# Kernel tuning notes

Hardware: AMD Instinct MI355X
Metric: run time of the kernel (lower is better)

The kernel has to match this reference:

```python
import jax, jax.numpy as jnp
import numpy as np

NODE = 64
T = 256
M = 2048
IN_SCALE = 1.0


def setup_inputs() -> dict:
    key = jax.random.key(0)
    k1, k2, k3, k4 = jax.random.split(key, 4)
    # nn.Linear-like init: small weights so the 255-step recurrence is stable
    W = jax.random.normal(k1, (T, NODE, NODE), dtype=jnp.float32) * 0.06
    b = jax.random.normal(k2, (T, NODE), dtype=jnp.float32) * 0.01
    noise_embedding = jnp.ones((1, NODE, T), dtype=jnp.float32)
    eps0 = jax.random.normal(k3, (M, NODE), dtype=jnp.float32)   # initial rsample noise
    eps = jax.random.normal(k4, (T - 1, M, NODE), dtype=jnp.float32)  # per-step noise, t=1..T-1
    return {"W": W, "b": b, "noise_embedding": noise_embedding, "eps0": eps0, "eps": eps}


def reference(W, b, noise_embedding, eps0, eps):
    m = eps0.shape[0]
    dtype = eps0.dtype
    m0 = jnp.zeros((m, NODE), dtype)
    s0 = jnp.full((m, NODE), IN_SCALE, dtype)
    x0 = s0 * eps0  # Normal(m0, s0).rsample()

    st_all = jax.nn.softplus(noise_embedding[0].T)  # (T, NODE)

    def step(x_prev, inp):
        Wt, bt, st, et = inp
        mt = x_prev @ Wt.T + bt                       # (M, NODE) coupling layer
        s_full = jnp.broadcast_to(st, (m, NODE))      # repeat over batch
        xt = mt + s_full * et
        return xt, (xt, mt, s_full)

    _, (xs, ms, ss) = jax.lax.scan(step, x0, (W[1:], b[1:], st_all[1:], eps))

    def pack(first, rest):
        seq = jnp.concatenate([first[None], rest], axis=0)  # (T, M, NODE), t ascending
        return jnp.flip(seq, axis=0).transpose(1, 2, 0)     # (M, NODE, T), reversed order

    return pack(x0, xs), pack(m0, ms), pack(s0, ss)
```

## Files before the change

### kernel.cpp

```cpp
#include <hip/hip_runtime.h>
#include <cmath>


typedef __bf16 bf16x8 __attribute__((ext_vector_type(8)));
typedef float f32x4 __attribute__((ext_vector_type(4)));

#define XB_STRIDE 144

__device__ __forceinline__ float softplus_f(float z) {
  return (z > 20.0f) ? z : log1pf(expf(z));
}

__global__ void k_wf(const float* __restrict__ W, const float* __restrict__ ne,
                     bf16x8* __restrict__ Wf, float* __restrict__ st,
                     float* __restrict__ stT) {
  int t = blockIdx.x;
  for (int e = threadIdx.x; e < 512; e += blockDim.x) {
    int lane = e & 63;
    int kh = (e >> 6) & 1;
    int nt = e >> 7;
    int q = lane >> 4, n15 = lane & 15;
    int n = nt * 16 + n15;
    int k0 = kh * 32 + q * 8;
    const float* src = W + ((size_t)t * 64 + n) * 64 + k0;
    bf16x8 v;
#pragma unroll
    for (int j = 0; j < 8; ++j) v[j] = (__bf16)src[j];
    Wf[((size_t)(t * 4 + nt) * 2 + kh) * 64 + lane] = v;
  }
  if (threadIdx.x < 64) {
    int n = threadIdx.x;
    float v = (t == 0) ? 1.0f : softplus_f(ne[n * 256 + t]);
    st[n * 256 + t] = v;
    stT[t * 64 + n] = v;
  }
}

__global__ __launch_bounds__(256) void k_prefix(const bf16x8* __restrict__ Wf,
                                                bf16x8* __restrict__ Pf) {
  __shared__ __align__(16) unsigned char Q[64 * XB_STRIDE];
  int b = blockIdx.x;
  int c = b + 1;
  int tid = threadIdx.x;
  int lane = tid & 63, w = tid >> 6;
  int q = lane >> 4, n15 = lane & 15;
  int rbase = w * 16;
  for (int e = tid; e < 4096; e += 256) {
    int r = e >> 6, k = e & 63;
    *(__bf16*)(Q + r * XB_STRIDE + k * 2) = (__bf16)((r == k) ? 1.0f : 0.0f);
  }
  __syncthreads();
  for (int tl = 0; tl < 16; ++tl) {
    int t = c * 16 + tl;
    bf16x8 a0 = *(const bf16x8*)(Q + (rbase + n15) * XB_STRIDE + q * 16);
    bf16x8 a1 = *(const bf16x8*)(Q + (rbase + n15) * XB_STRIDE + 64 + q * 16);
    f32x4 acc[4];
#pragma unroll
    for (int nt = 0; nt < 4; ++nt) {
      bf16x8 b0 = Wf[((size_t)(t * 4 + nt) * 2 + 0) * 64 + lane];
      bf16x8 b1 = Wf[((size_t)(t * 4 + nt) * 2 + 1) * 64 + lane];
      f32x4 z = {0.f, 0.f, 0.f, 0.f};
      z = __builtin_amdgcn_mfma_f32_16x16x32_bf16(a0, b0, z, 0, 0, 0);
      z = __builtin_amdgcn_mfma_f32_16x16x32_bf16(a1, b1, z, 0, 0, 0);
      acc[nt] = z;
    }
#pragma unroll
    for (int nt = 0; nt < 4; ++nt)
#pragma unroll
      for (int reg = 0; reg < 4; ++reg)
        *(__bf16*)(Q + (rbase + 4 * q + reg) * XB_STRIDE + (nt * 16 + n15) * 2) =
            (__bf16)acc[nt][reg];
    __syncthreads();
    for (int e = tid; e < 512; e += 256) {
      int lane2 = e & 63;
      int kh = (e >> 6) & 1;
      int nt = e >> 7;
      int q2 = lane2 >> 4;
      int nn = nt * 16 + (lane2 & 15);
      bf16x8 v;
#pragma unroll
      for (int j = 0; j < 8; ++j)
        v[j] = *(const __bf16*)(Q + (kh * 32 + q2 * 8 + j) * XB_STRIDE + nn * 2);
      Pf[((size_t)(b * 16 + tl) * 8 + nt * 2 + kh) * 64 + lane2] = v;
    }
    __syncthreads();
  }
}

__global__ __launch_bounds__(256) void k_phase1(
    const float* __restrict__ bb, const float* __restrict__ st,
    const float* __restrict__ eps0, const float* __restrict__ eps,
    const bf16x8* __restrict__ Wf, float* __restrict__ xtemp) {
  __shared__ float stab[16][64];
  __shared__ float btab[16][64];
  __shared__ __align__(16) unsigned char xball[4 * 16 * XB_STRIDE];
  int tid = threadIdx.x, w = tid >> 6, lane = tid & 63;
  unsigned char* xb = xball + w * 16 * XB_STRIDE;
  int c = blockIdx.x >> 5;
  int r0 = ((blockIdx.x & 31) * 4 + w) * 16;
  int q = lane >> 4, n15 = lane & 15;
  for (int e = tid; e < 1024; e += 256) {
    int tl = e >> 6, n = e & 63, t = c * 16 + tl;
    stab[tl][n] = st[n * 256 + t];
    btab[tl][n] = bb[t * 64 + n];
  }
  if (c == 0) {
    for (int i = 0; i < 16; ++i) {
      float v = eps0[(size_t)(r0 + i) * 64 + lane];
      *(__bf16*)(xb + i * XB_STRIDE + lane * 2) = (__bf16)v;
      xtemp[((size_t)(r0 + i)) * 64 + lane] = v;
    }
  } else {
    for (int i = 0; i < 16; ++i)
      *(__bf16*)(xb + i * XB_STRIDE + lane * 2) = (__bf16)0.0f;
  }
  __syncthreads();
  int t0 = (c == 0) ? 1 : c * 16;
  int t1 = c * 16 + 15;
  float epc[16], epn[16];
#pragma unroll
  for (int nt = 0; nt < 4; ++nt)
#pragma unroll
    for (int reg = 0; reg < 4; ++reg)
      epc[nt * 4 + reg] =
          eps[((size_t)(t0 - 1) * 2048 + r0 + 4 * q + reg) * 64 + nt * 16 + n15];
  for (int t = t0; t <= t1; ++t) {
    bool more = (t < t1);
    if (more) {
#pragma unroll
      for (int nt = 0; nt < 4; ++nt)
#pragma unroll
        for (int reg = 0; reg < 4; ++reg)
          epn[nt * 4 + reg] =
              eps[((size_t)t * 2048 + r0 + 4 * q + reg) * 64 + nt * 16 + n15];
    }
    bf16x8 a0 = *(const bf16x8*)(xb + n15 * XB_STRIDE + q * 16);
    bf16x8 a1 = *(const bf16x8*)(xb + n15 * XB_STRIDE + 64 + q * 16);
    f32x4 acc[4];
#pragma unroll
    for (int nt = 0; nt < 4; ++nt) {
      bf16x8 b0 = Wf[((size_t)(t * 4 + nt) * 2 + 0) * 64 + lane];
      bf16x8 b1 = Wf[((size_t)(t * 4 + nt) * 2 + 1) * 64 + lane];
      f32x4 z = {0.f, 0.f, 0.f, 0.f};
      z = __builtin_amdgcn_mfma_f32_16x16x32_bf16(a0, b0, z, 0, 0, 0);
      z = __builtin_amdgcn_mfma_f32_16x16x32_bf16(a1, b1, z, 0, 0, 0);
      acc[nt] = z;
    }
    int tl = t - c * 16;
#pragma unroll
    for (int nt = 0; nt < 4; ++nt) {
      int n = nt * 16 + n15;
      float sv = stab[tl][n];
      float bv = btab[tl][n];
#pragma unroll
      for (int reg = 0; reg < 4; ++reg) {
        int row = 4 * q + reg;
        float xn = acc[nt][reg] + bv + sv * epc[nt * 4 + reg];
        xtemp[((size_t)t * 2048 + r0 + row) * 64 + n] = xn;
        *(__bf16*)(xb + row * XB_STRIDE + n * 2) = (__bf16)xn;
      }
    }
    if (more) {
#pragma unroll
      for (int i = 0; i < 16; ++i) epc[i] = epn[i];
    }
  }
}

__global__ __launch_bounds__(256) void k_phase2(const bf16x8* __restrict__ Pf,
                                                const float* __restrict__ xtemp,
                                                bf16x8* __restrict__ hA) {
  __shared__ __align__(16) unsigned char hball[4 * 16 * XB_STRIDE];
  int tid = threadIdx.x, w = tid >> 6, lane = tid & 63;
  unsigned char* hb = hball + w * 16 * XB_STRIDE;
  int rtile = blockIdx.x * 4 + w;
  int r0 = rtile * 16;
  int q = lane >> 4, n15 = lane & 15;
  for (int i = 0; i < 16; ++i) {
    float v = xtemp[((size_t)15 * 2048 + r0 + i) * 64 + lane];
    *(__bf16*)(hb + i * XB_STRIDE + lane * 2) = (__bf16)v;
  }
  for (int c = 1; c <= 15; ++c) {
    bf16x8 a0 = *(const bf16x8*)(hb + n15 * XB_STRIDE + q * 16);
    bf16x8 a1 = *(const bf16x8*)(hb + n15 * XB_STRIDE + 64 + q * 16);
    size_t hbase = ((size_t)(c - 1) * 128 + rtile) * 128;
    hA[hbase + lane] = a0;
    hA[hbase + 64 + lane] = a1;
    if (c == 15) break;
    f32x4 acc[4];
#pragma unroll
    for (int nt = 0; nt < 4; ++nt) {
      bf16x8 b0 = Pf[((size_t)((c - 1) * 16 + 15) * 8 + nt * 2 + 0) * 64 + lane];
      bf16x8 b1 = Pf[((size_t)((c - 1) * 16 + 15) * 8 + nt * 2 + 1) * 64 + lane];
      f32x4 z = {0.f, 0.f, 0.f, 0.f};
      z = __builtin_amdgcn_mfma_f32_16x16x32_bf16(a0, b0, z, 0, 0, 0);
      z = __builtin_amdgcn_mfma_f32_16x16x32_bf16(a1, b1, z, 0, 0, 0);
      acc[nt] = z;
    }
#pragma unroll
    for (int nt = 0; nt < 4; ++nt) {
      int n = nt * 16 + n15;
#pragma unroll
      for (int reg = 0; reg < 4; ++reg) {
        int row = 4 * q + reg;
        float tail = xtemp[((size_t)(16 * c + 15) * 2048 + r0 + row) * 64 + n];
        float hn = acc[nt][reg] + tail;
        *(__bf16*)(hb + row * XB_STRIDE + n * 2) = (__bf16)hn;
      }
    }
  }
}

__global__ __launch_bounds__(256) void k_fix(const bf16x8* __restrict__ Pf,
                                             const bf16x8* __restrict__ hA,
                                             float* __restrict__ xtemp) {
  int tid = threadIdx.x, w = tid >> 6, lane = tid & 63;
  int rtile = (blockIdx.x & 31) * 4 + w;
  int r0 = rtile * 16;
  int ct = blockIdx.x >> 5;
  int c1 = ct >> 4;
  int tl = ct & 15;
  int c = c1 + 1;
  int t = 16 * c + tl;
  int q = lane >> 4, n15 = lane & 15;
  size_t hbase = ((size_t)c1 * 128 + rtile) * 128;
  bf16x8 a0 = hA[hbase + lane];
  bf16x8 a1 = hA[hbase + 64 + lane];
#pragma unroll
  for (int nt = 0; nt < 4; ++nt) {
    bf16x8 b0 = Pf[((size_t)(c1 * 16 + tl) * 8 + nt * 2 + 0) * 64 + lane];
    bf16x8 b1 = Pf[((size_t)(c1 * 16 + tl) * 8 + nt * 2 + 1) * 64 + lane];
    f32x4 z = {0.f, 0.f, 0.f, 0.f};
    z = __builtin_amdgcn_mfma_f32_16x16x32_bf16(a0, b0, z, 0, 0, 0);
    z = __builtin_amdgcn_mfma_f32_16x16x32_bf16(a1, b1, z, 0, 0, 0);
#pragma unroll
    for (int reg = 0; reg < 4; ++reg) {
      size_t idx = ((size_t)t * 2048 + r0 + 4 * q + reg) * 64 + nt * 16 + n15;
      xtemp[idx] += z[reg];
    }
  }
}

__global__ __launch_bounds__(256) void k_pack(const float* __restrict__ stT,
                                              const float* __restrict__ eps0,
                                              const float* __restrict__ eps,
                                              const float* __restrict__ xtemp,
                                              float* __restrict__ out) {
  __shared__ __align__(16) float lds[4][64 * 36];
  int tid = threadIdx.x;
  int w = tid >> 6, lane = tid & 63;
  float* wls = lds[w];
  int task = blockIdx.x * 4 + w;
  int tile = task >> 11;
  int mm = task & 2047;
  int tt0 = tile * 32;
  int iblk0 = 224 - tt0;
  int l15 = lane & 15, L = lane >> 4;
  int n0 = 4 * l15;
  f32x4 xr[8], er[8];
#pragma unroll
  for (int r = 0; r < 8; ++r) {
    int t = tt0 + 4 * r + L;
    xr[r] = *(const f32x4*)(xtemp + ((size_t)t * 2048 + mm) * 64 + n0);
    const float* erow = (t == 0) ? (eps0 + (size_t)mm * 64)
                                 : (eps + ((size_t)(t - 1) * 2048 + mm) * 64);
    er[r] = *(const f32x4*)(erow + n0);
  }
#pragma unroll
  for (int r = 0; r < 8; ++r) {
    int t = tt0 + 4 * r + L;
    f32x4 s = *(const f32x4*)(stT + (size_t)t * 64 + n0);
    er[r] = xr[r] - s * er[r];
  }
  int nrd = lane >> 3;
  int crd = (lane & 7) * 4;
  const size_t MSOFF = (size_t)2048 * 64 * 256;
  size_t obase = ((size_t)mm * 64) * 256 + (size_t)(iblk0 + crd);
#pragma unroll
  for (int r = 0; r < 8; ++r) {
    int col = 31 - 4 * r - L;
#pragma unroll
    for (int j = 0; j < 4; ++j) wls[(n0 + j) * 36 + col] = xr[r][j];
  }
#pragma unroll
  for (int jj = 0; jj < 8; ++jj) {
    int nn = 8 * jj + nrd;
    f32x4 v = *(const f32x4*)(wls + nn * 36 + crd);
    *(f32x4*)(out + obase + (size_t)nn * 256) = v;
  }
#pragma unroll
  for (int r = 0; r < 8; ++r) {
    int col = 31 - 4 * r - L;
#pragma unroll
    for (int j = 0; j < 4; ++j) wls[(n0 + j) * 36 + col] = er[r][j];
  }
#pragma unroll
  for (int jj = 0; jj < 8; ++jj) {
    int nn = 8 * jj + nrd;
    f32x4 v = *(const f32x4*)(wls + nn * 36 + crd);
    *(f32x4*)(out + MSOFF + obase + (size_t)nn * 256) = v;
  }
}

__global__ __launch_bounds__(256) void k_s(const float* __restrict__ st,
                                           float* __restrict__ out) {
  int gid = blockIdx.x * 256 + threadIdx.x;
  int i0 = (gid & 63) * 4;
  int n = (gid >> 6) & 63;
  int m = gid >> 12;
  const float4 rv = *(const float4*)(st + n * 256 + 252 - i0);
  f32x4 v = {rv.w, rv.z, rv.y, rv.x};
  *(f32x4*)(out + (size_t)2 * 2048 * 64 * 256 + ((size_t)m * 64 + n) * 256 + i0) = v;
}

extern "C" void kernel_launch(void* const* d_in, const int* in_sizes, int n_in,
                              void* d_out, int out_size, void* d_ws, size_t ws_size,
                              hipStream_t stream) {
  const float* W = (const float*)d_in[0];
  const float* bb = (const float*)d_in[1];
  const float* ne = (const float*)d_in[2];
  const float* eps0 = (const float*)d_in[3];
  const float* eps = (const float*)d_in[4];
  float* out = (float*)d_out;
  char* ws = (char*)d_ws;
  bf16x8* Wf = (bf16x8*)ws;
  float* st = (float*)(ws + (size_t)(2u << 20));
  float* stT = (float*)(ws + (size_t)(2u << 20) + (128u << 10));
  bf16x8* Pf = (bf16x8*)(ws + (size_t)(2u << 20) + (256u << 10));
  bf16x8* hA = (bf16x8*)(ws + (size_t)(4u << 20) + (256u << 10));
  float* xtemp = out + (size_t)2 * 2048 * 64 * 256;

  hipLaunchKernelGGL(k_wf, dim3(256), dim3(256), 0, stream, W, ne, Wf, st, stT);
  hipLaunchKernelGGL(k_prefix, dim3(15), dim3(256), 0, stream, Wf, Pf);
  hipLaunchKernelGGL(k_phase1, dim3(512), dim3(256), 0, stream, bb, st, eps0, eps, Wf, xtemp);
  hipLaunchKernelGGL(k_phase2, dim3(32), dim3(256), 0, stream, Pf, xtemp, hA);
  hipLaunchKernelGGL(k_fix, dim3(7680), dim3(256), 0, stream, Pf, hA, xtemp);
  hipLaunchKernelGGL(k_pack, dim3(4096), dim3(256), 0, stream, stT, eps0, eps, xtemp, out);
  hipLaunchKernelGGL(k_s, dim3(32768), dim3(256), 0, stream, st, out);
}
```

Baseline: 673.3 us.

## Stage MFMA outputs through swizzled LDS for coalesced 16-byte global stores

In phase1 and the fix kernel, MFMA accumulator outputs are first written to a per-wave XOR-swizzled LDS tile and then read back so each lane writes contiguous float4 rows to xtemp. The fix kernel now does a vectorized read-modify-write instead of scattered scalar +=. The pack kernel replaces its padded LDS transpose with an XOR-swizzled layout and scalar LDS reads. The aim is fewer, wider global memory transactions and fewer LDS bank conflicts, at the cost of extra LDS traffic, larger shared memory use, and possibly lower occupancy.

```diff
diff --git a/kernel.cpp b/kernel.cpp
--- a/kernel.cpp
+++ b/kernel.cpp
@@ -6,6 +6,9 @@
 typedef float f32x4 __attribute__((ext_vector_type(4)));
 
 #define XB_STRIDE 144
+
+#define SWA(row, col) ((row)*64 + ((col) ^ ((((row)) & 7) << 2)))
+#define SWP(row, col) ((row)*32 + ((col) ^ ((((row) >> 2) & 7) << 2)))
 
 __device__ __forceinline__ float softplus_f(float z) {
   return (z > 20.0f) ? z : log1pf(expf(z));
@@ -94,8 +97,10 @@
   __shared__ float stab[16][64];
   __shared__ float btab[16][64];
   __shared__ __align__(16) unsigned char xball[4 * 16 * XB_STRIDE];
+  __shared__ __align__(16) float xstage[4][16 * 64];
   int tid = threadIdx.x, w = tid >> 6, lane = tid & 63;
   unsigned char* xb = xball + w * 16 * XB_STRIDE;
+  float* xs = xstage[w];
   int c = blockIdx.x >> 5;
   int r0 = ((blockIdx.x & 31) * 4 + w) * 16;
   int q = lane >> 4, n15 = lane & 15;
@@ -156,10 +161,24 @@
       for (int reg = 0; reg < 4; ++reg) {
         int row = 4 * q + reg;
         float xn = acc[nt][reg] + bv + sv * epc[nt * 4 + reg];
-        xtemp[((size_t)t * 2048 + r0 + row) * 64 + n] = xn;
+        xs[SWA(row, n)] = xn;
         *(__bf16*)(xb + row * XB_STRIDE + n * 2) = (__bf16)xn;
       }
     }
+    asm volatile("" ::: "memory");
+    {
+      size_t basef = ((size_t)t * 2048 + r0) * 64 + 4 * lane;
+#pragma unroll
+      for (int k = 0; k < 4; ++k) {
+        int rr = 4 * k + (lane >> 4);
+        int cc = 4 * (lane & 15);
+        f32x4 v;
+#pragma unroll
+        for (int j = 0; j < 4; ++j) v[j] = xs[SWA(rr, cc + j)];
+        *(f32x4*)(xtemp + basef + 256 * k) = v;
+      }
+    }
+    asm volatile("" ::: "memory");
     if (more) {
 #pragma unroll
       for (int i = 0; i < 16; ++i) epc[i] = epn[i];
@@ -214,7 +233,9 @@
 __global__ __launch_bounds__(256) void k_fix(const bf16x8* __restrict__ Pf,
                                              const bf16x8* __restrict__ hA,
                                              float* __restrict__ xtemp) {
+  __shared__ __align__(16) float cst[4][16 * 64];
   int tid = threadIdx.x, w = tid >> 6, lane = tid & 63;
+  float* cs = cst[w];
   int rtile = (blockIdx.x & 31) * 4 + w;
   int r0 = rtile * 16;
   int ct = blockIdx.x >> 5;
@@ -234,10 +255,21 @@
     z = __builtin_amdgcn_mfma_f32_16x16x32_bf16(a0, b0, z, 0, 0, 0);
     z = __builtin_amdgcn_mfma_f32_16x16x32_bf16(a1, b1, z, 0, 0, 0);
 #pragma unroll
-    for (int reg = 0; reg < 4; ++reg) {
-      size_t idx = ((size_t)t * 2048 + r0 + 4 * q + reg) * 64 + nt * 16 + n15;
-      xtemp[idx] += z[reg];
-    }
+    for (int reg = 0; reg < 4; ++reg)
+      cs[SWA(4 * q + reg, nt * 16 + n15)] = z[reg];
+  }
+  asm volatile("" ::: "memory");
+  size_t basef = ((size_t)t * 2048 + r0) * 64 + 4 * lane;
+#pragma unroll
+  for (int k = 0; k < 4; ++k) {
+    int rr = 4 * k + (lane >> 4);
+    int cc = 4 * (lane & 15);
+    f32x4 cv;
+#pragma unroll
+    for (int j = 0; j < 4; ++j) cv[j] = cs[SWA(rr, cc + j)];
+    f32x4 xv = *(const f32x4*)(xtemp + basef + 256 * k);
+    xv += cv;
+    *(f32x4*)(xtemp + basef + 256 * k) = xv;
   }
 }
 
@@ -246,7 +278,7 @@
                                               const float* __restrict__ eps,
                                               const float* __restrict__ xtemp,
                                               float* __restrict__ out) {
-  __shared__ __align__(16) float lds[4][64 * 36];
+  __shared__ __align__(16) float lds[4][64 * 32];
   int tid = threadIdx.x;
   int w = tid >> 6, lane = tid & 63;
   float* wls = lds[w];
@@ -280,24 +312,31 @@
   for (int r = 0; r < 8; ++r) {
     int col = 31 - 4 * r - L;
 #pragma unroll
-    for (int j = 0; j < 4; ++j) wls[(n0 + j) * 36 + col] = xr[r][j];
-  }
+    for (int j = 0; j < 4; ++j) wls[SWP(n0 + j, col)] = xr[r][j];
+  }
+  asm volatile("" ::: "memory");
 #pragma unroll
   for (int jj = 0; jj < 8; ++jj) {
     int nn = 8 * jj + nrd;
-    f32x4 v = *(const f32x4*)(wls + nn * 36 + crd);
+    f32x4 v;
+#pragma unroll
+    for (int j = 0; j < 4; ++j) v[j] = wls[SWP(nn, crd + j)];
     *(f32x4*)(out + obase + (size_t)nn * 256) = v;
   }
+  asm volatile("" ::: "memory");
 #pragma unroll
   for (int r = 0; r < 8; ++r) {
     int col = 31 - 4 * r - L;
 #pragma unroll
-    for (int j = 0; j < 4; ++j) wls[(n0 + j) * 36 + col] = er[r][j];
-  }
+    for (int j = 0; j < 4; ++j) wls[SWP(n0 + j, col)] = er[r][j];
+  }
+  asm volatile("" ::: "memory");
 #pragma unroll
   for (int jj = 0; jj < 8; ++jj) {
     int nn = 8 * jj + nrd;
-    f32x4 v = *(const f32x4*)(wls + nn * 36 + crd);
+    f32x4 v;
+#pragma unroll
+    for (int j = 0; j < 4; ++j) v[j] = wls[SWP(nn, crd + j)];
     *(f32x4*)(out + MSOFF + obase + (size_t)nn * 256) = v;
   }
 }
```

Measured after the change: 664.2 us. About the same (-1.3%).
